# Kernel optimization log

Measured on AMD Instinct MI355X. Metric: run time of the kernel, lower is better.

## Reference

```python
import jax, jax.numpy as jnp
import numpy as np

D = 128
N = {'atom': 200000, 'bond': 200000, 'global': 4000}
# (short_name, src_type, dst_type, num_edges) -- order matches param index axis
ETS = [('a2b', 'atom', 'bond', 400000),
       ('b2a', 'bond', 'atom', 400000),
       ('a2g', 'atom', 'global', 200000),
       ('g2a', 'global', 'atom', 200000),
       ('b2g', 'bond', 'global', 200000),
       ('g2b', 'global', 'bond', 200000),
       ('a2a', 'atom', 'atom', 400000),
       ('b2b', 'bond', 'bond', 400000),
       ('g2g', 'global', 'global', 4000)]
N_LAYERS = 2
BN_EPS = 1e-5


def setup_inputs() -> dict:
    key = jax.random.key(0)
    ks = jax.random.split(key, 32)
    inp = {}
    inp['x_atom'] = jax.random.normal(ks[0], (N['atom'], D), jnp.float32)
    inp['x_bond'] = jax.random.normal(ks[1], (N['bond'], D), jnp.float32)
    inp['x_global'] = jax.random.normal(ks[2], (N['global'], D), jnp.float32)
    for i, (name, s, d, E) in enumerate(ETS):
        k1, k2 = jax.random.split(ks[3 + i])
        src = jax.random.randint(k1, (E,), 0, N[s], dtype=jnp.int32)
        dst = jax.random.randint(k2, (E,), 0, N[d], dtype=jnp.int32)
        inp['ei_' + name] = jnp.stack([src, dst])  # (2, E)
    scale = 0.05
    inp['W_rel'] = jax.random.normal(ks[20], (N_LAYERS, 9, D, D), jnp.float32) * scale
    inp['b_rel'] = jnp.zeros((N_LAYERS, 9, D), jnp.float32)
    inp['W_root'] = jax.random.normal(ks[21], (N_LAYERS, 9, D, D), jnp.float32) * scale
    inp['gamma'] = jnp.ones((N_LAYERS, 9, D), jnp.float32)
    inp['beta'] = jnp.zeros((N_LAYERS, 9, D), jnp.float32)
    return inp


def _conv(x_src, x_dst, ei, Wr, br, Wo, g, b):
    # PyG GraphConv(aggr='add'): lin_rel(sum of neighbor msgs) + lin_root(x_dst)
    agg = jax.ops.segment_sum(x_src[ei[0]], ei[1], num_segments=x_dst.shape[0])  # (N_dst, D)
    h = agg @ Wr + br + x_dst @ Wo
    # BatchNorm1d, training-mode batch statistics (biased variance, as torch)
    mu = h.mean(axis=0)
    var = h.var(axis=0)
    return g * (h - mu) * jax.lax.rsqrt(var + BN_EPS) + b


def _forward(xd, eid, W_rel, b_rel, W_root, gamma, beta):
    resid = xd
    for L in range(N_LAYERS):
        out = {k: jnp.zeros_like(v) for k, v in xd.items()}
        for i, (name, s, d, _) in enumerate(ETS):
            out[d] = out[d] + _conv(xd[s], xd[d], eid[name],
                                    W_rel[L, i], b_rel[L, i], W_root[L, i],
                                    gamma[L, i], beta[L, i])
        xd = out
    # residual add (not output block)
    return {k: xd[k] + resid[k] for k in xd}


def reference(x_atom, x_bond, x_global, W_rel, b_rel, W_root, gamma, beta,
              ei_a2b, ei_b2a, ei_a2g, ei_g2a, ei_b2g, ei_g2b, ei_a2a, ei_b2b, ei_g2g):
    eid = {'a2b': ei_a2b, 'b2a': ei_b2a, 'a2g': ei_a2g, 'g2a': ei_g2a,
           'b2g': ei_b2g, 'g2b': ei_g2b, 'a2a': ei_a2a, 'b2b': ei_b2b, 'g2g': ei_g2g}
    xd = {'atom': x_atom, 'bond': x_bond, 'global': x_global}
    out = _forward(xd, eid, W_rel, b_rel, W_root, gamma, beta)
    return (out['atom'], out['bond'], out['global'])
```

## Files before the change

### kernel.cpp

```cpp
#include <hip/hip_runtime.h>
#include <hip/hip_bf16.h>

typedef __bf16 bf16x8 __attribute__((ext_vector_type(8)));
typedef float  f32x4  __attribute__((ext_vector_type(4)));

#define SCHUNK 2048

struct EdgeArgs {
    const int* ei[9];
    int E[9];
    int ebase[10];
    int binbase[9];
};

struct ConvGroup {
    const int* rowptr[3];
    const __bf16* xsrc[3];
    const __bf16* agg[3];
    const __bf16* Wp[3];
    const float* bias[3];
    float* stats[3];
    __bf16* hout[3];
    const __bf16* xdst;
    const int* csr;
    int fused[3];
    int M;
};

struct NormGroup {
    const __bf16* h[3];
    const float* stats[3];
    const float* gamma[3];
    const float* beta[3];
    const float* resid;
    void* out;
    float invM;
    int M;
};

__global__ void __launch_bounds__(256) pack_w(const float* __restrict__ Wrel,
                                              const float* __restrict__ Wroot,
                                              __bf16* __restrict__ Wp)
{
    const int idx = blockIdx.x * 256 + threadIdx.x;
    if (idx >= 2 * 9 * 8 * 8 * 64) return;
    const int lane = idx & 63;
    int t = idx >> 6;
    const int cf = t & 7; t >>= 3;
    const int ks = t & 7; t >>= 3;
    const int li = t;
    const int col = cf * 16 + (lane & 15);
    const int kb  = ks * 32 + (lane >> 4) * 8;
    bf16x8 o;
#pragma unroll
    for (int j = 0; j < 8; ++j) {
        const int k = kb + j;
        const float v = (k < 128)
            ? Wrel [((size_t)li * 128 + k)        * 128 + col]
            : Wroot[((size_t)li * 128 + (k - 128)) * 128 + col];
        o[j] = (__bf16)v;
    }
    *reinterpret_cast<bf16x8*>(Wp + (size_t)idx * 8) = o;
}

__global__ void __launch_bounds__(256) cvt_kernel(const float* __restrict__ in,
                                                  __bf16* __restrict__ out, int n8)
{
    int i = blockIdx.x * 256 + threadIdx.x;
    const int stride = gridDim.x * 256;
    for (; i < n8; i += stride) {
        const float4 f0 = *reinterpret_cast<const float4*>(in + (size_t)i * 8);
        const float4 f1 = *reinterpret_cast<const float4*>(in + (size_t)i * 8 + 4);
        bf16x8 o;
        o[0] = (__bf16)f0.x; o[1] = (__bf16)f0.y; o[2] = (__bf16)f0.z; o[3] = (__bf16)f0.w;
        o[4] = (__bf16)f1.x; o[5] = (__bf16)f1.y; o[6] = (__bf16)f1.z; o[7] = (__bf16)f1.w;
        *reinterpret_cast<bf16x8*>(out + (size_t)i * 8) = o;
    }
}

__global__ void __launch_bounds__(256) hist_kernel(EdgeArgs ea, int Etot,
                                                   int* __restrict__ deg)
{
    int g = blockIdx.x * 256 + threadIdx.x;
    const int stride = gridDim.x * 256;
    for (; g < Etot; g += stride) {
        int t = 0;
        while (g >= ea.ebase[t + 1]) ++t;
        const int e = g - ea.ebase[t];
        const int dst = __builtin_nontemporal_load(&ea.ei[t][ea.E[t] + e]);
        atomicAdd(&deg[ea.binbase[t] + dst], 1);
    }
}

__global__ void __launch_bounds__(256) scan1_kernel(const int* __restrict__ deg, int n,
                                                    int* __restrict__ rowptr,
                                                    int* __restrict__ bsum)
{
    __shared__ int lds[256];
    const int tid = threadIdx.x;
    const int base = blockIdx.x * SCHUNK + tid * 8;
    int v[8]; int tsum = 0;
#pragma unroll
    for (int j = 0; j < 8; ++j) { v[j] = (base + j < n) ? deg[base + j] : 0; tsum += v[j]; }
    int incl = tsum;
    lds[tid] = incl; __syncthreads();
    for (int off = 1; off < 256; off <<= 1) {
        const int add = (tid >= off) ? lds[tid - off] : 0;
        __syncthreads();
        incl += add; lds[tid] = incl; __syncthreads();
    }
    if (tid == 255) bsum[blockIdx.x] = incl;
    int run = incl - tsum;
#pragma unroll
    for (int j = 0; j < 8; ++j) { if (base + j < n) rowptr[base + j] = run; run += v[j]; }
}

__global__ void __launch_bounds__(256) scan2_kernel(int* __restrict__ bsum, int nb)
{
    __shared__ int lds[256];
    __shared__ int carry_s;
    const int tid = threadIdx.x;
    if (tid == 0) carry_s = 0;
    __syncthreads();
    for (int base = 0; base < nb; base += 256) {
        const int v = (base + tid < nb) ? bsum[base + tid] : 0;
        int incl = v;
        lds[tid] = incl; __syncthreads();
        for (int off = 1; off < 256; off <<= 1) {
            const int add = (tid >= off) ? lds[tid - off] : 0;
            __syncthreads();
            incl += add; lds[tid] = incl; __syncthreads();
        }
        const int total = lds[255];
        const int carry = carry_s;
        if (base + tid < nb) bsum[base + tid] = incl - v + carry;
        __syncthreads();
        if (tid == 0) carry_s = carry + total;
        __syncthreads();
    }
}

__global__ void __launch_bounds__(256) fixup_kernel(int* __restrict__ rowptr,
                                                    const int* __restrict__ bsum, int n,
                                                    int Etot, int* __restrict__ cursor)
{
    int i = blockIdx.x * 256 + threadIdx.x;
    const int stride = gridDim.x * 256;
    if (i == 0) rowptr[n] = Etot;
    for (; i < n; i += stride) {
        const int r = rowptr[i] + bsum[i >> 11];
        rowptr[i] = r; cursor[i] = r;
    }
}

__global__ void __launch_bounds__(256) place_kernel(EdgeArgs ea, int Etot, int Nbins,
                                                    int* __restrict__ cursor,
                                                    int* __restrict__ csr)
{
    const int shard = blockIdx.x & 7;
    const int lo = (int)(((long long)shard * Nbins) >> 3);
    const int hi = (int)(((long long)(shard + 1) * Nbins) >> 3);
    int g = (blockIdx.x >> 3) * 256 + threadIdx.x;
    const int stride = (gridDim.x >> 3) * 256;
    for (; g < Etot; g += stride) {
        int t = 0;
        while (g >= ea.ebase[t + 1]) ++t;
        const int e = g - ea.ebase[t];
        const int dst = __builtin_nontemporal_load(&ea.ei[t][ea.E[t] + e]);
        const int gb = ea.binbase[t] + dst;
        if (gb >= lo && gb < hi) {
            const int src = __builtin_nontemporal_load(&ea.ei[t][e]);
            const int pos = atomicAdd(&cursor[gb], 1);
            csr[pos] = src;
        }
    }
}

__global__ void __launch_bounds__(256) gather64(const __bf16* __restrict__ x,
                                                const int* __restrict__ rowptr,
                                                const int* __restrict__ csr,
                                                __bf16* __restrict__ agg, int N)
{
    const int lane = threadIdx.x & 63;
    const int l16 = lane & 15, grp = lane >> 4;
    int wv = (blockIdx.x * 256 + threadIdx.x) >> 6;
    const int nwv = (gridDim.x * 256) >> 6;
    for (int row = wv; row < N; row += nwv) {
        const int p0 = rowptr[row], p1 = rowptr[row + 1];
        float acc[8] = {0.f, 0.f, 0.f, 0.f, 0.f, 0.f, 0.f, 0.f};
        int p = p0 + grp * 2;
        for (; p + 2 <= p1; p += 8) {
            const int s0 = csr[p], s1 = csr[p + 1];
            const bf16x8 v0 = *reinterpret_cast<const bf16x8*>(x + (size_t)s0 * 128 + l16 * 8);
            const bf16x8 v1 = *reinterpret_cast<const bf16x8*>(x + (size_t)s1 * 128 + l16 * 8);
#pragma unroll
            for (int j = 0; j < 8; ++j) acc[j] += (float)v0[j] + (float)v1[j];
        }
        if (p < p1) {
            const int s0 = csr[p];
            const bf16x8 v0 = *reinterpret_cast<const bf16x8*>(x + (size_t)s0 * 128 + l16 * 8);
#pragma unroll
            for (int j = 0; j < 8; ++j) acc[j] += (float)v0[j];
        }
#pragma unroll
        for (int j = 0; j < 8; ++j) {
            acc[j] += __shfl_xor(acc[j], 16);
            acc[j] += __shfl_xor(acc[j], 32);
        }
        if (grp == 0) {
            bf16x8 o;
#pragma unroll
            for (int j = 0; j < 8; ++j) o[j] = (__bf16)acc[j];
            *reinterpret_cast<bf16x8*>(agg + (size_t)row * 128 + l16 * 8) = o;
        }
    }
}

__global__ void __launch_bounds__(256, 3) fgemm_group(ConvGroup cg)
{
    __shared__ __bf16 atile[128 * 128];
    __shared__ float lsum[128];
    __shared__ float lsq[128];
    const int cj   = blockIdx.y;
    const int M    = cg.M;
    const int tid  = threadIdx.x;
    const int lane = tid & 63;
    const int wv   = tid >> 6;
    if (tid < 128) { lsum[tid] = 0.f; lsq[tid] = 0.f; }

    const int r0 = blockIdx.x * 128;
    const int lrow  = lane & 15;
    const int klane = (lane >> 4) * 8;

    int  car[2]; bool val[2];
#pragma unroll
    for (int rf = 0; rf < 2; ++rf) {
        const int ar = r0 + wv * 32 + rf * 16 + lrow;
        val[rf] = ar < M;
        car[rf] = val[rf] ? ar : (M - 1);
    }
    bf16x8 z8;
#pragma unroll
    for (int j = 0; j < 8; ++j) z8[j] = (__bf16)0.f;

    bf16x8 xd[2][4];
#pragma unroll
    for (int rf = 0; rf < 2; ++rf)
#pragma unroll
        for (int kk = 0; kk < 4; ++kk) {
            const bf16x8 av = *reinterpret_cast<const bf16x8*>(
                cg.xdst + (size_t)car[rf] * 128 + kk * 32 + klane);
            xd[rf][kk] = val[rf] ? av : z8;
        }

    const bool fused = cg.fused[cj] != 0;
    if (fused) {
        const int* __restrict__ rp  = cg.rowptr[cj];
        const int* __restrict__ csr = cg.csr;
        const __bf16* __restrict__ xsrc = cg.xsrc[cj];
        const int grp = tid >> 4, l16 = tid & 15;
        int pr[9];
#pragma unroll
        for (int rr = 0; rr < 9; ++rr) {
            int rw = r0 + grp * 8 + rr;
            pr[rr] = rp[rw > M ? M : rw];
        }
#pragma unroll
        for (int rr = 0; rr < 8; ++rr) {
            const int lr = grp * 8 + rr;
            const int p1 = pr[rr + 1];
            float acc[8] = {0.f, 0.f, 0.f, 0.f, 0.f, 0.f, 0.f, 0.f};
            int p = pr[rr];
            for (; p + 2 <= p1; p += 2) {
                const int s0 = csr[p], s1 = csr[p + 1];
                const bf16x8 v0 = *reinterpret_cast<const bf16x8*>(
                    xsrc + (size_t)s0 * 128 + l16 * 8);
                const bf16x8 v1 = *reinterpret_cast<const bf16x8*>(
                    xsrc + (size_t)s1 * 128 + l16 * 8);
#pragma unroll
                for (int j = 0; j < 8; ++j) acc[j] += (float)v0[j] + (float)v1[j];
            }
            if (p < p1) {
                const int s0 = csr[p];
                const bf16x8 v0 = *reinterpret_cast<const bf16x8*>(
                    xsrc + (size_t)s0 * 128 + l16 * 8);
#pragma unroll
                for (int j = 0; j < 8; ++j) acc[j] += (float)v0[j];
            }
            bf16x8 o;
#pragma unroll
            for (int j = 0; j < 8; ++j) o[j] = (__bf16)acc[j];
            char* dp = (char*)atile + lr * 256 + ((l16 * 16) ^ ((lr & 7) << 4));
            *reinterpret_cast<bf16x8*>(dp) = o;
        }
    }
    __syncthreads();

    f32x4 acc[2][8];
#pragma unroll
    for (int rf = 0; rf < 2; ++rf)
#pragma unroll
        for (int cf = 0; cf < 8; ++cf) {
            f32x4 z; z[0] = 0.f; z[1] = 0.f; z[2] = 0.f; z[3] = 0.f;
            acc[rf][cf] = z;
        }

    const __bf16* __restrict__ aggp = cg.agg[cj];
    const __bf16* __restrict__ Wp   = cg.Wp[cj];
#pragma unroll
    for (int ks = 0; ks < 8; ++ks) {
        const int koff = (ks & 3) * 32 + klane;
        bf16x8 a[2];
#pragma unroll
        for (int rf = 0; rf < 2; ++rf) {
            if (ks < 4) {
                if (fused) {
                    const int lr = wv * 32 + rf * 16 + lrow;
                    const char* sp = (const char*)atile + lr * 256
                                   + ((koff * 2) ^ ((lr & 7) << 4));
                    a[rf] = *reinterpret_cast<const bf16x8*>(sp);
                } else {
                    const bf16x8 av = *reinterpret_cast<const bf16x8*>(
                        aggp + (size_t)car[rf] * 128 + koff);
                    a[rf] = val[rf] ? av : z8;
                }
            } else {
                a[rf] = xd[rf][ks - 4];
            }
        }
        const bf16x8* wp8 = reinterpret_cast<const bf16x8*>(Wp) + (size_t)ks * 8 * 64 + lane;
        bf16x8 b[8];
#pragma unroll
        for (int cf = 0; cf < 8; ++cf) b[cf] = wp8[(size_t)cf * 64];
#pragma unroll
        for (int rf = 0; rf < 2; ++rf)
#pragma unroll
            for (int cf = 0; cf < 8; ++cf)
                acc[rf][cf] = __builtin_amdgcn_mfma_f32_16x16x32_bf16(a[rf], b[cf], acc[rf][cf], 0, 0, 0);
    }

    const float* __restrict__ bias = cg.bias[cj];
    __bf16* __restrict__ hout = cg.hout[cj];
    float bc[8];
#pragma unroll
    for (int cf = 0; cf < 8; ++cf) bc[cf] = bias[cf * 16 + lrow];

    const int rb = (lane >> 4) * 4;
#pragma unroll
    for (int cf = 0; cf < 8; ++cf) {
        float s = 0.f, q = 0.f;
#pragma unroll
        for (int rf = 0; rf < 2; ++rf) {
#pragma unroll
            for (int rr = 0; rr < 4; ++rr) {
                const int grow = r0 + wv * 32 + rf * 16 + rb + rr;
                if (grow < M) {
                    const float hv = acc[rf][cf][rr] + bc[cf];
                    hout[(size_t)grow * 128 + cf * 16 + lrow] = (__bf16)hv;
                    s += hv; q += hv * hv;
                }
            }
        }
        s += __shfl_xor(s, 16); s += __shfl_xor(s, 32);
        q += __shfl_xor(q, 16); q += __shfl_xor(q, 32);
        if (lane < 16) {
            atomicAdd(&lsum[cf * 16 + lane], s);
            atomicAdd(&lsq [cf * 16 + lane], q);
        }
    }
    __syncthreads();
    float* __restrict__ st = cg.stats[cj];
    if (tid < 128) {
        atomicAdd(&st[tid],       lsum[tid]);
        atomicAdd(&st[128 + tid], lsq[tid]);
    }
}

template<bool F32OUT>
__global__ void __launch_bounds__(256) norm_group(NormGroup ng)
{
    __shared__ float ssc[3][128], ssh[3][128];
    const int tid = threadIdx.x;
    if (tid < 128) {
#pragma unroll
        for (int j = 0; j < 3; ++j) {
            const float mu   = ng.stats[j][tid] * ng.invM;
            const float var  = ng.stats[j][128 + tid] * ng.invM - mu * mu;
            const float scal = ng.gamma[j][tid] * rsqrtf(var + 1e-5f);
            ssc[j][tid] = scal;
            ssh[j][tid] = ng.beta[j][tid] - mu * scal;
        }
    }
    __syncthreads();

    const int t0   = blockIdx.x * 256 + tid;
    const int nthr = gridDim.x * 256;
    const int c0   = (t0 & 15) * 8;
    float sc[3][8], sh[3][8];
#pragma unroll
    for (int j = 0; j < 3; ++j)
#pragma unroll
        for (int k = 0; k < 8; ++k) { sc[j][k] = ssc[j][c0 + k]; sh[j][k] = ssh[j][c0 + k]; }

    const int nch = ng.M * 16;
    for (int ch = t0; ch < nch; ch += nthr) {
        float f[8] = {0.f, 0.f, 0.f, 0.f, 0.f, 0.f, 0.f, 0.f};
#pragma unroll
        for (int j = 0; j < 3; ++j) {
            const bf16x8 hv = *reinterpret_cast<const bf16x8*>(ng.h[j] + (size_t)ch * 8);
#pragma unroll
            for (int k = 0; k < 8; ++k) f[k] += (float)hv[k] * sc[j][k] + sh[j][k];
        }
        if constexpr (F32OUT) {
            const float* rp = ng.resid + (size_t)ch * 8;
            const float4 r0 = *reinterpret_cast<const float4*>(rp);
            const float4 r1 = *reinterpret_cast<const float4*>(rp + 4);
            float* op = (float*)ng.out + (size_t)ch * 8;
            float4 o0, o1;
            o0.x = r0.x + f[0]; o0.y = r0.y + f[1]; o0.z = r0.z + f[2]; o0.w = r0.w + f[3];
            o1.x = r1.x + f[4]; o1.y = r1.y + f[5]; o1.z = r1.z + f[6]; o1.w = r1.w + f[7];
            *reinterpret_cast<float4*>(op)     = o0;
            *reinterpret_cast<float4*>(op + 4) = o1;
        } else {
            bf16x8 ov;
#pragma unroll
            for (int k = 0; k < 8; ++k) ov[k] = (__bf16)f[k];
            *reinterpret_cast<bf16x8*>((__bf16*)ng.out + (size_t)ch * 8) = ov;
        }
    }
}

extern "C" void kernel_launch(void* const* d_in, const int* in_sizes, int n_in,
                              void* d_out, int out_size, void* d_ws, size_t ws_size,
                              hipStream_t stream)
{
    const float* xin[3] = {(const float*)d_in[0], (const float*)d_in[1], (const float*)d_in[2]};
    const int N[3] = {in_sizes[0] / 128, in_sizes[1] / 128, in_sizes[2] / 128};
    const float* Wrel  = (const float*)d_in[12];
    const float* brel  = (const float*)d_in[13];
    const float* Wroot = (const float*)d_in[14];
    const float* gamma = (const float*)d_in[15];
    const float* beta  = (const float*)d_in[16];

    const int cs[9] = {0, 1, 0, 2, 1, 2, 0, 1, 2};
    const int cd[9] = {1, 0, 2, 0, 2, 1, 0, 1, 2};
    const int gconv[3][3] = {{1, 3, 6},
                             {0, 5, 7},
                             {2, 4, 8}};

    const size_t nA = (size_t)N[0] * 128, nB = (size_t)N[1] * 128, nG = (size_t)N[2] * 128;
    const size_t off[3] = {0, nA, nA + nB};
    const size_t xtot = nA + nB + nG;
    size_t maxN = (size_t)N[0];
    if ((size_t)N[1] > maxN) maxN = N[1];
    if ((size_t)N[2] > maxN) maxN = N[2];

    EdgeArgs ea;
    int Etot = 0, Nbins = 0;
    ea.ebase[0] = 0;
    for (int t = 0; t < 9; ++t) {
        ea.ei[t] = (const int*)d_in[3 + t];
        ea.E[t]  = in_sizes[3 + t] / 2;
        ea.ebase[t + 1] = ea.ebase[t] + ea.E[t];
        ea.binbase[t] = Nbins;
        Nbins += N[cd[t]];
    }
    Etot = ea.ebase[9];
    const int nb1 = (Nbins + SCHUNK - 1) / SCHUNK;

    auto al = [](size_t x) { return (x + 15) & ~(size_t)15; };
    char* w = (char*)d_ws;
    __bf16* x0b   = (__bf16*)w;  w += al(xtot * 2);
    __bf16* x1    = (__bf16*)w;  w += al(xtot * 2);
    __bf16* aggb  = (__bf16*)w;  w += al(2 * maxN * 128 * 2);
    __bf16* hbuf  = (__bf16*)w;  w += al(3 * maxN * 128 * 2);
    float*  stats = (float*)w;   w += al(18 * 256 * 4);
    __bf16* Wp    = (__bf16*)w;  w += al((size_t)18 * 32768 * 2);
    int*    deg   = (int*)w;     w += al((size_t)Nbins * 4);
    int*    rowptr= (int*)w;     w += al(((size_t)Nbins + 1) * 4);
    int*    cursor= (int*)w;     w += al((size_t)Nbins * 4);
    int*    csr   = (int*)w;     w += al((size_t)Etot * 4);
    int*    bsum  = (int*)w;     w += al((size_t)nb1 * 4);
    (void)ws_size; (void)n_in; (void)out_size;

    pack_w<<<288, 256, 0, stream>>>(Wrel, Wroot, Wp);
    for (int k = 0; k < 3; ++k) {
        const int n8 = (int)(((k == 0 ? nA : k == 1 ? nB : nG)) / 8);
        int cb = (n8 + 255) / 256; if (cb > 2048) cb = 2048;
        cvt_kernel<<<cb, 256, 0, stream>>>(xin[k], x0b + off[k], n8);
    }
    hipMemsetAsync(deg, 0, (size_t)Nbins * 4, stream);
    hipMemsetAsync(stats, 0, 18 * 256 * 4, stream);

    int eb = (Etot + 255) / 256; if (eb > 2048) eb = 2048;
    hist_kernel<<<eb, 256, 0, stream>>>(ea, Etot, deg);
    scan1_kernel<<<nb1, 256, 0, stream>>>(deg, Nbins, rowptr, bsum);
    scan2_kernel<<<1, 256, 0, stream>>>(bsum, nb1);
    int fb = (Nbins + 255) / 256; if (fb > 2048) fb = 2048;
    fixup_kernel<<<fb, 256, 0, stream>>>(rowptr, bsum, Nbins, Etot, cursor);
    place_kernel<<<2048, 256, 0, stream>>>(ea, Etot, Nbins, cursor, csr);

    float* dout = (float*)d_out;

    for (int L = 0; L < 2; ++L) {
        const __bf16* xb = (L == 0) ? x0b : x1;

        {
            const int Ng = N[2];
            int gb2 = (Ng * 64 + 255) / 256; if (gb2 > 2048) gb2 = 2048; if (gb2 < 1) gb2 = 1;
            gather64<<<gb2, 256, 0, stream>>>(xb + off[0], rowptr + ea.binbase[2], csr,
                                              aggb, Ng);
            gather64<<<gb2, 256, 0, stream>>>(xb + off[1], rowptr + ea.binbase[4], csr,
                                              aggb + maxN * 128, Ng);
        }

        for (int g = 0; g < 3; ++g) {
            const int d  = g;
            const int Nd = N[d];
            ConvGroup cg;
            NormGroup ng;
            cg.xdst = xb + off[d];
            cg.csr  = csr;
            cg.M    = Nd;
            for (int j = 0; j < 3; ++j) {
                const int et = gconv[g][j];
                const int li = L * 9 + et;
                cg.rowptr[j] = rowptr + ea.binbase[et];
                cg.xsrc[j]   = xb + off[cs[et]];
                cg.Wp[j]     = Wp + (size_t)li * 32768;
                cg.bias[j]   = brel + li * 128;
                cg.stats[j]  = stats + li * 256;
                cg.hout[j]   = hbuf + (size_t)j * maxN * 128;
                const bool hi = (et == 2) || (et == 4);
                cg.fused[j]  = hi ? 0 : 1;
                cg.agg[j]    = (et == 2) ? aggb : (et == 4 ? aggb + maxN * 128 : (const __bf16*)nullptr);
                ng.h[j]      = cg.hout[j];
                ng.stats[j]  = cg.stats[j];
                ng.gamma[j]  = gamma + li * 128;
                ng.beta[j]   = beta + li * 128;
            }
            const int gb = (Nd + 127) / 128;
            fgemm_group<<<dim3(gb, 3), 256, 0, stream>>>(cg);

            ng.invM = 1.0f / (float)Nd;
            ng.M    = Nd;
            const long long nch = (long long)Nd * 16;
            int nb = (int)((nch + 255) / 256); if (nb > 2048) nb = 2048;
            if (L == 0) {
                ng.resid = nullptr;
                ng.out   = (void*)(x1 + off[d]);
                norm_group<false><<<nb, 256, 0, stream>>>(ng);
            } else {
                ng.resid = xin[d];
                ng.out   = (void*)(dout + off[d]);
                norm_group<true><<<nb, 256, 0, stream>>>(ng);
            }
        }
    }
}
```

Baseline: 1.547 ms.

## Edge-parallel fused aggregation with fp32 LDS atomics and src/dst CSR pairs

The CSR now stores (src, dst) int pairs. The fused GEMM kernel's aggregation changes from row-by-row per 16-lane group to edge-parallel over the block's whole edge range, accumulating into an fp32 shared-memory tile with LDS atomics. The A operand is then converted to bf16 as it is loaded. The aim is to fix the load imbalance from variable node degrees. In exchange, CSR traffic doubles, the LDS tile doubles in size (occupancy drops from 3 to 2 blocks), and LDS atomic contention is added.

```diff
diff --git a/kernel.cpp b/kernel.cpp
--- a/kernel.cpp
+++ b/kernel.cpp
@@ -22,7 +22,7 @@
     float* stats[3];
     __bf16* hout[3];
     const __bf16* xdst;
-    const int* csr;
+    const int2* csr2;
     int fused[3];
     int M;
 };
@@ -155,7 +155,7 @@
 
 __global__ void __launch_bounds__(256) place_kernel(EdgeArgs ea, int Etot, int Nbins,
                                                     int* __restrict__ cursor,
-                                                    int* __restrict__ csr)
+                                                    int2* __restrict__ csr2)
 {
     const int shard = blockIdx.x & 7;
     const int lo = (int)(((long long)shard * Nbins) >> 3);
@@ -171,14 +171,14 @@
         if (gb >= lo && gb < hi) {
             const int src = __builtin_nontemporal_load(&ea.ei[t][e]);
             const int pos = atomicAdd(&cursor[gb], 1);
-            csr[pos] = src;
+            csr2[pos] = make_int2(src, dst);
         }
     }
 }
 
 __global__ void __launch_bounds__(256) gather64(const __bf16* __restrict__ x,
                                                 const int* __restrict__ rowptr,
-                                                const int* __restrict__ csr,
+                                                const int2* __restrict__ csr2,
                                                 __bf16* __restrict__ agg, int N)
 {
     const int lane = threadIdx.x & 63;
@@ -190,14 +190,14 @@
         float acc[8] = {0.f, 0.f, 0.f, 0.f, 0.f, 0.f, 0.f, 0.f};
         int p = p0 + grp * 2;
         for (; p + 2 <= p1; p += 8) {
-            const int s0 = csr[p], s1 = csr[p + 1];
+            const int s0 = csr2[p].x, s1 = csr2[p + 1].x;
             const bf16x8 v0 = *reinterpret_cast<const bf16x8*>(x + (size_t)s0 * 128 + l16 * 8);
             const bf16x8 v1 = *reinterpret_cast<const bf16x8*>(x + (size_t)s1 * 128 + l16 * 8);
 #pragma unroll
             for (int j = 0; j < 8; ++j) acc[j] += (float)v0[j] + (float)v1[j];
         }
         if (p < p1) {
-            const int s0 = csr[p];
+            const int s0 = csr2[p].x;
             const bf16x8 v0 = *reinterpret_cast<const bf16x8*>(x + (size_t)s0 * 128 + l16 * 8);
 #pragma unroll
             for (int j = 0; j < 8; ++j) acc[j] += (float)v0[j];
@@ -216,9 +216,9 @@
     }
 }
 
-__global__ void __launch_bounds__(256, 3) fgemm_group(ConvGroup cg)
-{
-    __shared__ __bf16 atile[128 * 128];
+__global__ void __launch_bounds__(256, 2) fgemm_group(ConvGroup cg)
+{
+    __shared__ float ftile[128 * 132];
     __shared__ float lsum[128];
     __shared__ float lsq[128];
     const int cj   = blockIdx.y;
@@ -226,7 +226,6 @@
     const int tid  = threadIdx.x;
     const int lane = tid & 63;
     const int wv   = tid >> 6;
-    if (tid < 128) { lsum[tid] = 0.f; lsq[tid] = 0.f; }
 
     const int r0 = blockIdx.x * 128;
     const int lrow  = lane & 15;
@@ -253,45 +252,43 @@
             xd[rf][kk] = val[rf] ? av : z8;
         }
 
+    if (tid < 128) { lsum[tid] = 0.f; lsq[tid] = 0.f; }
+
     const bool fused = cg.fused[cj] != 0;
     if (fused) {
-        const int* __restrict__ rp  = cg.rowptr[cj];
-        const int* __restrict__ csr = cg.csr;
+        f32x4 zz; zz[0] = 0.f; zz[1] = 0.f; zz[2] = 0.f; zz[3] = 0.f;
+        for (int i = tid; i < 128 * 132 / 4; i += 256)
+            *reinterpret_cast<f32x4*>(ftile + i * 4) = zz;
+        __syncthreads();
+
+        const int* __restrict__ rp = cg.rowptr[cj];
+        const int2* __restrict__ cs2 = cg.csr2;
         const __bf16* __restrict__ xsrc = cg.xsrc[cj];
         const int grp = tid >> 4, l16 = tid & 15;
-        int pr[9];
-#pragma unroll
-        for (int rr = 0; rr < 9; ++rr) {
-            int rw = r0 + grp * 8 + rr;
-            pr[rr] = rp[rw > M ? M : rw];
-        }
-#pragma unroll
-        for (int rr = 0; rr < 8; ++rr) {
-            const int lr = grp * 8 + rr;
-            const int p1 = pr[rr + 1];
-            float acc[8] = {0.f, 0.f, 0.f, 0.f, 0.f, 0.f, 0.f, 0.f};
-            int p = pr[rr];
-            for (; p + 2 <= p1; p += 2) {
-                const int s0 = csr[p], s1 = csr[p + 1];
-                const bf16x8 v0 = *reinterpret_cast<const bf16x8*>(
-                    xsrc + (size_t)s0 * 128 + l16 * 8);
-                const bf16x8 v1 = *reinterpret_cast<const bf16x8*>(
-                    xsrc + (size_t)s1 * 128 + l16 * 8);
-#pragma unroll
-                for (int j = 0; j < 8; ++j) acc[j] += (float)v0[j] + (float)v1[j];
-            }
-            if (p < p1) {
-                const int s0 = csr[p];
-                const bf16x8 v0 = *reinterpret_cast<const bf16x8*>(
-                    xsrc + (size_t)s0 * 128 + l16 * 8);
-#pragma unroll
-                for (int j = 0; j < 8; ++j) acc[j] += (float)v0[j];
-            }
-            bf16x8 o;
-#pragma unroll
-            for (int j = 0; j < 8; ++j) o[j] = (__bf16)acc[j];
-            char* dp = (char*)atile + lr * 256 + ((l16 * 16) ^ ((lr & 7) << 4));
-            *reinterpret_cast<bf16x8*>(dp) = o;
+        const int rend = (r0 + 128 < M) ? (r0 + 128) : M;
+        const int P0 = rp[r0], P1 = rp[rend];
+        int p = P0 + grp;
+        for (; p + 16 < P1; p += 32) {
+            const int2 e0 = cs2[p];
+            const int2 e1 = cs2[p + 16];
+            const bf16x8 v0 = *reinterpret_cast<const bf16x8*>(
+                xsrc + (size_t)e0.x * 128 + l16 * 8);
+            const bf16x8 v1 = *reinterpret_cast<const bf16x8*>(
+                xsrc + (size_t)e1.x * 128 + l16 * 8);
+            float* f0 = ftile + (e0.y - r0) * 132 + l16 * 8;
+            float* f1 = ftile + (e1.y - r0) * 132 + l16 * 8;
+#pragma unroll
+            for (int j = 0; j < 8; ++j) atomicAdd(f0 + j, (float)v0[j]);
+#pragma unroll
+            for (int j = 0; j < 8; ++j) atomicAdd(f1 + j, (float)v1[j]);
+        }
+        if (p < P1) {
+            const int2 e0 = cs2[p];
+            const bf16x8 v0 = *reinterpret_cast<const bf16x8*>(
+                xsrc + (size_t)e0.x * 128 + l16 * 8);
+            float* f0 = ftile + (e0.y - r0) * 132 + l16 * 8;
+#pragma unroll
+            for (int j = 0; j < 8; ++j) atomicAdd(f0 + j, (float)v0[j]);
         }
     }
     __syncthreads();
@@ -316,9 +313,15 @@
             if (ks < 4) {
                 if (fused) {
                     const int lr = wv * 32 + rf * 16 + lrow;
-                    const char* sp = (const char*)atile + lr * 256
-                                   + ((koff * 2) ^ ((lr & 7) << 4));
-                    a[rf] = *reinterpret_cast<const bf16x8*>(sp);
+                    const float* sp = ftile + lr * 132 + koff;
+                    const float4 a0 = *reinterpret_cast<const float4*>(sp);
+                    const float4 a1 = *reinterpret_cast<const float4*>(sp + 4);
+                    bf16x8 av;
+                    av[0] = (__bf16)a0.x; av[1] = (__bf16)a0.y;
+                    av[2] = (__bf16)a0.z; av[3] = (__bf16)a0.w;
+                    av[4] = (__bf16)a1.x; av[5] = (__bf16)a1.y;
+                    av[6] = (__bf16)a1.z; av[7] = (__bf16)a1.w;
+                    a[rf] = av;
                 } else {
                     const bf16x8 av = *reinterpret_cast<const bf16x8*>(
                         aggp + (size_t)car[rf] * 128 + koff);
@@ -479,7 +482,7 @@
     int*    deg   = (int*)w;     w += al((size_t)Nbins * 4);
     int*    rowptr= (int*)w;     w += al(((size_t)Nbins + 1) * 4);
     int*    cursor= (int*)w;     w += al((size_t)Nbins * 4);
-    int*    csr   = (int*)w;     w += al((size_t)Etot * 4);
+    int2*   csr2  = (int2*)w;    w += al((size_t)Etot * 8);
     int*    bsum  = (int*)w;     w += al((size_t)nb1 * 4);
     (void)ws_size; (void)n_in; (void)out_size;
 
@@ -498,7 +501,7 @@
     scan2_kernel<<<1, 256, 0, stream>>>(bsum, nb1);
     int fb = (Nbins + 255) / 256; if (fb > 2048) fb = 2048;
     fixup_kernel<<<fb, 256, 0, stream>>>(rowptr, bsum, Nbins, Etot, cursor);
-    place_kernel<<<2048, 256, 0, stream>>>(ea, Etot, Nbins, cursor, csr);
+    place_kernel<<<2048, 256, 0, stream>>>(ea, Etot, Nbins, cursor, csr2);
 
     float* dout = (float*)d_out;
 
@@ -508,9 +511,9 @@
         {
             const int Ng = N[2];
             int gb2 = (Ng * 64 + 255) / 256; if (gb2 > 2048) gb2 = 2048; if (gb2 < 1) gb2 = 1;
-            gather64<<<gb2, 256, 0, stream>>>(xb + off[0], rowptr + ea.binbase[2], csr,
+            gather64<<<gb2, 256, 0, stream>>>(xb + off[0], rowptr + ea.binbase[2], csr2,
                                               aggb, Ng);
-            gather64<<<gb2, 256, 0, stream>>>(xb + off[1], rowptr + ea.binbase[4], csr,
+            gather64<<<gb2, 256, 0, stream>>>(xb + off[1], rowptr + ea.binbase[4], csr2,
                                               aggb + maxN * 128, Ng);
         }
 
@@ -520,7 +523,7 @@
             ConvGroup cg;
             NormGroup ng;
             cg.xdst = xb + off[d];
-            cg.csr  = csr;
+            cg.csr2 = csr2;
             cg.M    = Nd;
             for (int j = 0; j < 3; ++j) {
                 const int et = gconv[g][j];
```

Measured after the change: 3.756 ms. 143% more time.
